# Kernel tuning notes

Measured on AMD Instinct MI355X. Metric: run time of the kernel, lower is better.

The kernel has to match this reference:

```python
import jax, jax.numpy as jnp
import numpy as np

N = 100000
E = 1600000
IN_C = 128
HID = 32
OUT_C = 32
HEADS = 4
NEG_SLOPE = 0.2


def setup_inputs() -> dict:
    key = jax.random.key(0)
    ks = jax.random.split(key, 8)
    x = jax.random.normal(ks[0], (N, IN_C), dtype=jnp.float32)
    edge_index = jax.random.randint(ks[1], (2, E), 0, N, dtype=jnp.int64)
    s = 0.1
    W1 = jax.random.normal(ks[2], (IN_C, HEADS * HID), dtype=jnp.float32) * s
    att_src1 = jax.random.normal(ks[3], (HEADS, HID), dtype=jnp.float32) * s
    att_dst1 = jax.random.normal(ks[4], (HEADS, HID), dtype=jnp.float32) * s
    W2 = jax.random.normal(ks[5], (HEADS * HID, HEADS * OUT_C), dtype=jnp.float32) * s
    att_src2 = jax.random.normal(ks[6], (HEADS, OUT_C), dtype=jnp.float32) * s
    att_dst2 = jax.random.normal(ks[7], (HEADS, OUT_C), dtype=jnp.float32) * s
    return {"x": x, "edge_index": edge_index, "W1": W1, "att_src1": att_src1,
            "att_dst1": att_dst1, "W2": W2, "att_src2": att_src2, "att_dst2": att_dst2}


def _gat_conv(x, src, dst, W, a_src, a_dst, heads, ch):
    # linear transform: [N, heads, ch]
    h = (x @ W).reshape(-1, heads, ch)
    # per-node attention logits [N, heads]
    al_src = jnp.sum(h * a_src, axis=-1)
    al_dst = jnp.sum(h * a_dst, axis=-1)
    # per-edge attention [E, heads]
    e = jax.nn.leaky_relu(al_src[src] + al_dst[dst], negative_slope=NEG_SLOPE)
    # segment softmax over incoming edges of each dst node
    m = jax.ops.segment_max(e, dst, num_segments=N)
    e = jnp.exp(e - m[dst])
    denom = jax.ops.segment_sum(e, dst, num_segments=N)
    alpha = e / (denom[dst] + 1e-16)
    # message + scatter-add aggregation
    msg = h[src] * alpha[:, :, None]          # [E, heads, ch]
    out = jax.ops.segment_sum(msg, dst, num_segments=N)
    return out.reshape(-1, heads * ch)        # concat heads (PyG default)


def reference(x, edge_index, W1, att_src1, att_dst1, W2, att_src2, att_dst2):
    # add self-loops (PyG GATConv default add_self_loops=True)
    loop = jnp.arange(N, dtype=edge_index.dtype)
    src = jnp.concatenate([edge_index[0], loop])
    dst = jnp.concatenate([edge_index[1], loop])
    h = _gat_conv(x, src, dst, W1, att_src1, att_dst1, HEADS, HID)
    h = jax.nn.relu(h)  # dropout is identity in eval mode
    out = _gat_conv(h, src, dst, W2, att_src2, att_dst2, HEADS, OUT_C)
    return out
```

## Files before the change

kernel.cpp:

```cpp
#include <hip/hip_runtime.h>

#define NN 100000
#define EE 1600000
#define NGRP 8
#define DRANGE 12500
#define SLOTS 48
#define NROWPAD 100032
#define NTILES 1563
#define PREP_BLK 50
#define BUILD_BLK 2048
#define GEMM_BLK 512

typedef short bf16x8 __attribute__((ext_vector_type(8)));
typedef float f32x4 __attribute__((ext_vector_type(4)));
typedef int   i32x4 __attribute__((ext_vector_type(4)));
typedef unsigned int u32x2 __attribute__((ext_vector_type(2)));

__device__ __forceinline__ float leaky(float x) { return x > 0.f ? x : 0.2f * x; }

__device__ __forceinline__ unsigned int bfpack2(float a, float b)
{
    unsigned int xa = __float_as_uint(a), xb = __float_as_uint(b);
    xa = (xa + 0x7fffu + ((xa >> 16) & 1u)) >> 16;
    xb = (xb + 0x7fffu + ((xb >> 16) & 1u)) & 0xffff0000u;
    return xa | xb;
}

__device__ __forceinline__ unsigned short bf1(float a)
{
    unsigned int x = __float_as_uint(a);
    return (unsigned short)((x + 0x7fffu + ((x >> 16) & 1u)) >> 16);
}

__device__ __forceinline__ float blo(unsigned int u) { return __uint_as_float(u << 16); }
__device__ __forceinline__ float bhi(unsigned int u) { return __uint_as_float(u & 0xffff0000u); }


__global__ __launch_bounds__(256) void prep_build(const float* __restrict__ W1, const float* __restrict__ W2,
                                                  unsigned short* __restrict__ Wtb1, unsigned short* __restrict__ Wtb2,
                                                  const float* __restrict__ as1, const float* __restrict__ ad1,
                                                  const float* __restrict__ as2, const float* __restrict__ ad2,
                                                  unsigned short* __restrict__ Wa1, unsigned short* __restrict__ Wa2,
                                                  unsigned int* __restrict__ Xbf,
                                                  const int* __restrict__ src, const int* __restrict__ dst,
                                                  int* __restrict__ cnt, int* __restrict__ csr)
{
    const int bid = blockIdx.x;
    if (bid < 32) {
        int tid = bid * 256 + threadIdx.x;
        int layer = tid >> 12;
        int rem = tid & 4095;
        int c = rem >> 5;
        int kq = (rem & 31) * 4;
        const float* Ws = layer ? W2 : W1;
        unsigned short* Wd = layer ? Wtb2 : Wtb1;
        ushort4 o;
        o.x = bf1(Ws[(kq + 0) * 128 + c]);
        o.y = bf1(Ws[(kq + 1) * 128 + c]);
        o.z = bf1(Ws[(kq + 2) * 128 + c]);
        o.w = bf1(Ws[(kq + 3) * 128 + c]);
        *(ushort4*)&Wd[c * 128 + kq] = o;
    } else if (bid < 48) {
        int tid = (bid - 32) * 256 + threadIdx.x;
        int layer = tid >> 11;
        int rem = tid & 2047;
        int col = rem >> 7;
        int k = rem & 127;
        const float* Ws = layer ? W2 : W1;
        unsigned short* Wd = layer ? Wa2 : Wa1;
        float s = 0.f;
        if (col < 8) {
            int head = col & 3;
            const float* av = (col < 4) ? (layer ? as2 : as1) : (layer ? ad2 : ad1);
            const float* wr = Ws + k * 128 + head * 32;
            const float* ar = av + head * 32;
            #pragma unroll
            for (int c = 0; c < 32; c++) s += wr[c] * ar[c];
        }
        Wd[col * 128 + k] = bf1(s);
    } else if (bid < PREP_BLK) {
        int t = (bid - 48) * 256 + threadIdx.x;
        ((uint4*)Xbf)[NN * 16 + t] = make_uint4(0, 0, 0, 0);
    } else {
        const int bb = bid - PREP_BLK;
        const int grp = bb & (NGRP - 1);
        const int gr  = bb >> 3;
        const int ng  = BUILD_BLK >> 3;
        const int dlo = grp * DRANGE, dhi = dlo + DRANGE;
        const int tid0 = gr * 256 + threadIdx.x;
        const int nthr = ng * 256;
        for (int e4 = tid0 * 4; e4 < EE; e4 += nthr * 4) {
            i32x4 dv = __builtin_nontemporal_load((const i32x4*)(dst + e4));
            i32x4 sv = __builtin_nontemporal_load((const i32x4*)(src + e4));
            #pragma unroll
            for (int j = 0; j < 4; ++j) {
                int d = dv[j];
                if (d >= dlo && d < dhi) {
                    int pos = atomicAdd(&cnt[d], 1);
                    if (pos < SLOTS) csr[(size_t)d * SLOTS + pos] = sv[j];
                }
            }
        }
    }
}


template<bool FP32IN>
__global__ __launch_bounds__(256) void gemm_mfma(const void* __restrict__ Xin,
                                                 const unsigned short* __restrict__ Wtb,
                                                 const unsigned short* __restrict__ Wa,
                                                 unsigned int* __restrict__ Hbf,
                                                 float* __restrict__ alS, float* __restrict__ alD)
{
    const int w = threadIdx.x >> 6, lane = threadIdx.x & 63;
    const int cl = lane & 15, b = lane >> 4;

    bf16x8 Bf[8][4];
    #pragma unroll
    for (int c = 0; c < 8; c++)
        #pragma unroll
        for (int s = 0; s < 4; s++)
            Bf[c][s] = *(const bf16x8*)(Wtb + (16 * c + cl) * 128 + 32 * s + 8 * b);

    bf16x8 Bf9[4];
    #pragma unroll
    for (int s = 0; s < 4; s++)
        Bf9[s] = *(const bf16x8*)(Wa + cl * 128 + 32 * s + 8 * b);

    for (int tile = blockIdx.x; tile < NTILES; tile += GEMM_BLK) {
        const int rowb = tile * 64 + 16 * w;
        const int rA = rowb + cl;
        bf16x8 Af[4];
        if constexpr (FP32IN) {
            if (rA < NN) {
                const float* pa = (const float*)Xin + (size_t)rA * 128 + 8 * b;
                #pragma unroll
                for (int s = 0; s < 4; s++) {
                    float4 f0 = *(const float4*)(pa + 32 * s);
                    float4 f1 = *(const float4*)(pa + 32 * s + 4);
                    union { bf16x8 v; unsigned int u[4]; } cv;
                    cv.u[0] = bfpack2(f0.x, f0.y); cv.u[1] = bfpack2(f0.z, f0.w);
                    cv.u[2] = bfpack2(f1.x, f1.y); cv.u[3] = bfpack2(f1.z, f1.w);
                    Af[s] = cv.v;
                }
            } else {
                union { bf16x8 v; unsigned int u[4]; } cz;
                cz.u[0] = cz.u[1] = cz.u[2] = cz.u[3] = 0;
                #pragma unroll
                for (int s = 0; s < 4; s++) Af[s] = cz.v;
            }
        } else {
            const unsigned short* pa = (const unsigned short*)Xin + (size_t)rA * 128 + 8 * b;
            #pragma unroll
            for (int s = 0; s < 4; s++) Af[s] = *(const bf16x8*)(pa + 32 * s);
        }

        f32x4 acc[8];
        #pragma unroll
        for (int c = 0; c < 8; c++) acc[c] = (f32x4){0.f, 0.f, 0.f, 0.f};
        f32x4 acc9 = (f32x4){0.f, 0.f, 0.f, 0.f};
        #pragma unroll
        for (int s = 0; s < 4; s++) {
            #pragma unroll
            for (int c = 0; c < 8; c++)
                acc[c] = __builtin_amdgcn_mfma_f32_16x16x32_bf16(Af[s], Bf[c][s], acc[c], 0, 0, 0);
            acc9 = __builtin_amdgcn_mfma_f32_16x16x32_bf16(Af[s], Bf9[s], acc9, 0, 0, 0);
        }

        const int row0 = rowb + 4 * b;
        #pragma unroll
        for (int c = 0; c < 8; c++) {
            #pragma unroll
            for (int r = 0; r < 4; r++) {
                float partner = __shfl_xor(acc[c][r], 1);
                if (!(cl & 1) && row0 + r < NN)
                    Hbf[(size_t)(row0 + r) * 64 + 8 * c + (cl >> 1)] = bfpack2(acc[c][r], partner);
            }
        }
        #pragma unroll
        for (int r = 0; r < 4; r++) {
            const int rr = row0 + r;
            if (rr < NN) {
                if (cl < 4)      alS[rr * 4 + cl] = acc9[r];
                else if (cl < 8) alD[rr * 4 + (cl - 4)] = acc9[r];
            }
        }
    }
}


__global__ __launch_bounds__(256) void agg_kernel(const unsigned int* __restrict__ Hbf,
                                                  const int* __restrict__ cnt, const int* __restrict__ csr,
                                                  const float* __restrict__ alS, const float* __restrict__ alD,
                                                  float* __restrict__ OUTf, unsigned int* __restrict__ OUTb,
                                                  int do_relu)
{
    __shared__ float pl[4][64 * 4];
    __shared__ int   sl[4][64];
    const int w = threadIdx.x >> 6, lane = threadIdx.x & 63;
    const int wid = (blockIdx.x * 256 + threadIdx.x) >> 6;
    if (wid >= NN) return;
    const int nreal = min(cnt[wid], SLOTS);
    const int nE = nreal + 1;
    const float4 ad = *(const float4*)&alD[wid * 4];
    const int half = lane >> 5, l5 = lane & 31;
    const int hq = l5 >> 3;
    const uint2* __restrict__ H2 = (const uint2*)Hbf + l5;
    const int* __restrict__ slots = csr + (size_t)wid * SLOTS;

    float4 acc = make_float4(0.f, 0.f, 0.f, 0.f);
    float den = 0.f;
    for (int base = 0; base < nE; base += 64) {
        const int nthis = min(64, nE - base);
        const int idx = base + lane;
        int s_ = 0;
        float4 p = make_float4(0.f, 0.f, 0.f, 0.f);
        if (lane < nthis) {
            s_ = (idx == nreal) ? wid : __builtin_nontemporal_load(slots + idx);
            float4 as = *(const float4*)&alS[s_ * 4];
            p.x = __expf(leaky(as.x + ad.x));
            p.y = __expf(leaky(as.y + ad.y));
            p.z = __expf(leaky(as.z + ad.z));
            p.w = __expf(leaky(as.w + ad.w));
        }
        sl[w][lane] = s_;
        *(float4*)&pl[w][lane * 4] = p;
        int k = 0;
        for (; k + 8 <= nthis; k += 8) {
            float p0 = pl[w][(k + half) * 4 + hq];
            float p1 = pl[w][(k + 2 + half) * 4 + hq];
            float p2 = pl[w][(k + 4 + half) * 4 + hq];
            float p3 = pl[w][(k + 6 + half) * 4 + hq];
            int s0i = sl[w][k + half];
            int s1i = sl[w][k + 2 + half];
            int s2i = sl[w][k + 4 + half];
            int s3i = sl[w][k + 6 + half];
            uint2 u0 = H2[(size_t)s0i * 32];
            uint2 u1 = H2[(size_t)s1i * 32];
            uint2 u2 = H2[(size_t)s2i * 32];
            uint2 u3 = H2[(size_t)s3i * 32];
            den += (p0 + p1) + (p2 + p3);
            acc.x += p0 * blo(u0.x); acc.y += p0 * bhi(u0.x);
            acc.z += p0 * blo(u0.y); acc.w += p0 * bhi(u0.y);
            acc.x += p1 * blo(u1.x); acc.y += p1 * bhi(u1.x);
            acc.z += p1 * blo(u1.y); acc.w += p1 * bhi(u1.y);
            acc.x += p2 * blo(u2.x); acc.y += p2 * bhi(u2.x);
            acc.z += p2 * blo(u2.y); acc.w += p2 * bhi(u2.y);
            acc.x += p3 * blo(u3.x); acc.y += p3 * bhi(u3.x);
            acc.z += p3 * blo(u3.y); acc.w += p3 * bhi(u3.y);
        }
        for (; k < nthis; k += 2) {
            float paf = pl[w][(k + half) * 4 + hq];
            int sa = sl[w][k + half];
            uint2 ua = H2[(size_t)sa * 32];
            den += paf;
            acc.x += paf * blo(ua.x); acc.y += paf * bhi(ua.x);
            acc.z += paf * blo(ua.y); acc.w += paf * bhi(ua.y);
        }
    }
    acc.x += __shfl_xor(acc.x, 32);
    acc.y += __shfl_xor(acc.y, 32);
    acc.z += __shfl_xor(acc.z, 32);
    acc.w += __shfl_xor(acc.w, 32);
    den   += __shfl_xor(den,   32);
    if (half == 0) {
        float inv = 1.f / (den + 1e-16f);
        float o0 = acc.x * inv, o1 = acc.y * inv, o2 = acc.z * inv, o3 = acc.w * inv;
        if (do_relu) {
            o0 = fmaxf(o0, 0.f); o1 = fmaxf(o1, 0.f);
            o2 = fmaxf(o2, 0.f); o3 = fmaxf(o3, 0.f);
        }
        if (OUTb) {
            u32x2 ov = { bfpack2(o0, o1), bfpack2(o2, o3) };
            __builtin_nontemporal_store(ov, (u32x2*)&OUTb[(size_t)wid * 64 + l5 * 2]);
        } else {
            f32x4 ov = { o0, o1, o2, o3 };
            __builtin_nontemporal_store(ov, (f32x4*)&OUTf[(size_t)wid * 128 + l5 * 4]);
        }
    }
}


extern "C" void kernel_launch(void* const* d_in, const int* in_sizes, int n_in,
                              void* d_out, int out_size, void* d_ws, size_t ws_size,
                              hipStream_t stream)
{
    const float* x   = (const float*)d_in[0];
    const int*   ei  = (const int*)d_in[1];
    const float* W1  = (const float*)d_in[2];
    const float* as1 = (const float*)d_in[3];
    const float* ad1 = (const float*)d_in[4];
    const float* W2  = (const float*)d_in[5];
    const float* as2 = (const float*)d_in[6];
    const float* ad2 = (const float*)d_in[7];
    const int* srcp = ei;
    const int* dstp = ei + EE;

    char* w = (char*)d_ws;
    unsigned int* Xbf  = (unsigned int*)w; w += (size_t)NROWPAD * 64 * 4;
    unsigned int* Hbf  = (unsigned int*)w; w += (size_t)NN * 64 * 4;
    unsigned short* Wtb1 = (unsigned short*)w; w += 16384 * 2;
    unsigned short* Wtb2 = (unsigned short*)w; w += 16384 * 2;
    unsigned short* Wa1  = (unsigned short*)w; w += 2048 * 2;
    unsigned short* Wa2  = (unsigned short*)w; w += 2048 * 2;
    float* alS = (float*)w; w += (size_t)NN * 4 * 4;
    float* alD = (float*)w; w += (size_t)NN * 4 * 4;
    int* cnt    = (int*)w;  w += (size_t)NN * 4;
    int* csr    = (int*)w;  w += (size_t)NN * SLOTS * 4;

    hipMemsetAsync(cnt, 0, NN * sizeof(int), stream);
    prep_build<<<PREP_BLK + BUILD_BLK, 256, 0, stream>>>(W1, W2, Wtb1, Wtb2,
                                                         as1, ad1, as2, ad2, Wa1, Wa2,
                                                         Xbf, srcp, dstp, cnt, csr);

    const int node_wave_blocks = (NN + 3) / 4;

    gemm_mfma<true><<<GEMM_BLK, 256, 0, stream>>>(x, Wtb1, Wa1, Hbf, alS, alD);
    agg_kernel<<<node_wave_blocks, 256, 0, stream>>>(Hbf, cnt, csr, alS, alD, nullptr, Xbf, 1);

    gemm_mfma<false><<<GEMM_BLK, 256, 0, stream>>>(Xbf, Wtb2, Wa2, Hbf, alS, alD);
    agg_kernel<<<node_wave_blocks, 256, 0, stream>>>(Hbf, cnt, csr, alS, alD, (float*)d_out, nullptr, 0);
}
```

Baseline: 288.9 us.

## Partition edges into destination buckets before CSR build; widen aggregation loads

The CSR build changes from each of 8 groups scanning all edges to a two-pass scheme. First, edges are partitioned into 8 destination-range buckets using shared-memory counters and one global atomic per bucket per block. A second kernel then fills the per-node slots from the bucketed edges. This cuts the 8x redundant reads of the edge list but adds an intermediate 64-bit edge buffer and an extra launch. Separately, the aggregation kernel now has each lane load 16 bytes (8 bf16 channels) with 4 edges in flight per wave, and it drops the outer loop beyond 64 edges, which assumes degree plus one never exceeds 64 (safe since SLOTS is 48).

```diff
diff --git a/kernel.cpp b/kernel.cpp
--- a/kernel.cpp
+++ b/kernel.cpp
@@ -8,13 +8,16 @@
 #define NROWPAD 100032
 #define NTILES 1563
 #define PREP_BLK 50
-#define BUILD_BLK 2048
+#define PART_BLK 512
+#define NITER 4
+#define EBCAP 225000
+#define BUILD2_BLK 2048
 #define GEMM_BLK 512
 
 typedef short bf16x8 __attribute__((ext_vector_type(8)));
 typedef float f32x4 __attribute__((ext_vector_type(4)));
 typedef int   i32x4 __attribute__((ext_vector_type(4)));
-typedef unsigned int u32x2 __attribute__((ext_vector_type(2)));
+typedef unsigned int u32x4 __attribute__((ext_vector_type(4)));
 
 __device__ __forceinline__ float leaky(float x) { return x > 0.f ? x : 0.2f * x; }
 
@@ -36,14 +39,14 @@
 __device__ __forceinline__ float bhi(unsigned int u) { return __uint_as_float(u & 0xffff0000u); }
 
 
-__global__ __launch_bounds__(256) void prep_build(const float* __restrict__ W1, const float* __restrict__ W2,
-                                                  unsigned short* __restrict__ Wtb1, unsigned short* __restrict__ Wtb2,
-                                                  const float* __restrict__ as1, const float* __restrict__ ad1,
-                                                  const float* __restrict__ as2, const float* __restrict__ ad2,
-                                                  unsigned short* __restrict__ Wa1, unsigned short* __restrict__ Wa2,
-                                                  unsigned int* __restrict__ Xbf,
-                                                  const int* __restrict__ src, const int* __restrict__ dst,
-                                                  int* __restrict__ cnt, int* __restrict__ csr)
+__global__ __launch_bounds__(256) void prep_part(const float* __restrict__ W1, const float* __restrict__ W2,
+                                                 unsigned short* __restrict__ Wtb1, unsigned short* __restrict__ Wtb2,
+                                                 const float* __restrict__ as1, const float* __restrict__ ad1,
+                                                 const float* __restrict__ as2, const float* __restrict__ ad2,
+                                                 unsigned short* __restrict__ Wa1, unsigned short* __restrict__ Wa2,
+                                                 unsigned int* __restrict__ Xbf,
+                                                 const int* __restrict__ src, const int* __restrict__ dst,
+                                                 int* __restrict__ bktcnt, unsigned long long* __restrict__ ebuf)
 {
     const int bid = blockIdx.x;
     if (bid < 32) {
@@ -82,25 +85,59 @@
         int t = (bid - 48) * 256 + threadIdx.x;
         ((uint4*)Xbf)[NN * 16 + t] = make_uint4(0, 0, 0, 0);
     } else {
+        __shared__ int lcnt[8];
+        __shared__ int lbase[8];
         const int bb = bid - PREP_BLK;
-        const int grp = bb & (NGRP - 1);
-        const int gr  = bb >> 3;
-        const int ng  = BUILD_BLK >> 3;
-        const int dlo = grp * DRANGE, dhi = dlo + DRANGE;
-        const int tid0 = gr * 256 + threadIdx.x;
-        const int nthr = ng * 256;
-        for (int e4 = tid0 * 4; e4 < EE; e4 += nthr * 4) {
-            i32x4 dv = __builtin_nontemporal_load((const i32x4*)(dst + e4));
-            i32x4 sv = __builtin_nontemporal_load((const i32x4*)(src + e4));
-            #pragma unroll
-            for (int j = 0; j < 4; ++j) {
-                int d = dv[j];
-                if (d >= dlo && d < dhi) {
-                    int pos = atomicAdd(&cnt[d], 1);
-                    if (pos < SLOTS) csr[(size_t)d * SLOTS + pos] = sv[j];
+        const int t = threadIdx.x;
+        const int nthr = PART_BLK * 256;
+        for (int it = 0; it < NITER; ++it) {
+            const int qidx = it * nthr + bb * 256 + t;
+            const bool valid = qidx < EE / 4;
+            if (t < 8) lcnt[t] = 0;
+            __syncthreads();
+            i32x4 dv, sv;
+            int g[4], pl_[4];
+            if (valid) {
+                dv = __builtin_nontemporal_load((const i32x4*)(dst + qidx * 4));
+                sv = __builtin_nontemporal_load((const i32x4*)(src + qidx * 4));
+                #pragma unroll
+                for (int j = 0; j < 4; ++j) {
+                    g[j] = dv[j] / DRANGE;
+                    pl_[j] = atomicAdd(&lcnt[g[j]], 1);
                 }
             }
-        }
+            __syncthreads();
+            if (t < 8) lbase[t] = atomicAdd(&bktcnt[t], lcnt[t]);
+            __syncthreads();
+            if (valid) {
+                #pragma unroll
+                for (int j = 0; j < 4; ++j) {
+                    int idx = lbase[g[j]] + pl_[j];
+                    ebuf[(size_t)g[j] * EBCAP + idx] =
+                        ((unsigned long long)(unsigned int)dv[j] << 32) | (unsigned int)sv[j];
+                }
+            }
+            __syncthreads();
+        }
+    }
+}
+
+
+__global__ __launch_bounds__(256) void build2_kernel(const int* __restrict__ bktcnt,
+                                                     const unsigned long long* __restrict__ ebuf,
+                                                     int* __restrict__ cnt, int* __restrict__ csr)
+{
+    const int g = blockIdx.x & (NGRP - 1);
+    const int gr = blockIdx.x >> 3;
+    const int ng = BUILD2_BLK >> 3;
+    const int n = bktcnt[g];
+    const unsigned long long* __restrict__ eb = ebuf + (size_t)g * EBCAP;
+    for (int i = gr * 256 + threadIdx.x; i < n; i += ng * 256) {
+        unsigned long long e = __builtin_nontemporal_load(eb + i);
+        int d = (int)(e >> 32);
+        int s = (int)(e & 0xffffffffu);
+        int pos = atomicAdd(&cnt[d], 1);
+        if (pos < SLOTS) csr[(size_t)d * SLOTS + pos] = s;
     }
 }
 
@@ -203,20 +240,19 @@
     const int nreal = min(cnt[wid], SLOTS);
     const int nE = nreal + 1;
     const float4 ad = *(const float4*)&alD[wid * 4];
-    const int half = lane >> 5, l5 = lane & 31;
-    const int hq = l5 >> 3;
-    const uint2* __restrict__ H2 = (const uint2*)Hbf + l5;
+    const int q = lane >> 4;
+    const int l4 = lane & 15;
+    const int hq = l4 >> 2;
+    const u32x4* __restrict__ H4 = (const u32x4*)Hbf + l4;
     const int* __restrict__ slots = csr + (size_t)wid * SLOTS;
 
-    float4 acc = make_float4(0.f, 0.f, 0.f, 0.f);
+    float a0 = 0.f, a1 = 0.f, a2 = 0.f, a3 = 0.f, a4 = 0.f, a5 = 0.f, a6 = 0.f, a7 = 0.f;
     float den = 0.f;
-    for (int base = 0; base < nE; base += 64) {
-        const int nthis = min(64, nE - base);
-        const int idx = base + lane;
+    {
         int s_ = 0;
         float4 p = make_float4(0.f, 0.f, 0.f, 0.f);
-        if (lane < nthis) {
-            s_ = (idx == nreal) ? wid : __builtin_nontemporal_load(slots + idx);
+        if (lane < nE) {
+            s_ = (lane == nreal) ? wid : __builtin_nontemporal_load(slots + lane);
             float4 as = *(const float4*)&alS[s_ * 4];
             p.x = __expf(leaky(as.x + ad.x));
             p.y = __expf(leaky(as.y + ad.y));
@@ -226,56 +262,61 @@
         sl[w][lane] = s_;
         *(float4*)&pl[w][lane * 4] = p;
         int k = 0;
-        for (; k + 8 <= nthis; k += 8) {
-            float p0 = pl[w][(k + half) * 4 + hq];
-            float p1 = pl[w][(k + 2 + half) * 4 + hq];
-            float p2 = pl[w][(k + 4 + half) * 4 + hq];
-            float p3 = pl[w][(k + 6 + half) * 4 + hq];
-            int s0i = sl[w][k + half];
-            int s1i = sl[w][k + 2 + half];
-            int s2i = sl[w][k + 4 + half];
-            int s3i = sl[w][k + 6 + half];
-            uint2 u0 = H2[(size_t)s0i * 32];
-            uint2 u1 = H2[(size_t)s1i * 32];
-            uint2 u2 = H2[(size_t)s2i * 32];
-            uint2 u3 = H2[(size_t)s3i * 32];
-            den += (p0 + p1) + (p2 + p3);
-            acc.x += p0 * blo(u0.x); acc.y += p0 * bhi(u0.x);
-            acc.z += p0 * blo(u0.y); acc.w += p0 * bhi(u0.y);
-            acc.x += p1 * blo(u1.x); acc.y += p1 * bhi(u1.x);
-            acc.z += p1 * blo(u1.y); acc.w += p1 * bhi(u1.y);
-            acc.x += p2 * blo(u2.x); acc.y += p2 * bhi(u2.x);
-            acc.z += p2 * blo(u2.y); acc.w += p2 * bhi(u2.y);
-            acc.x += p3 * blo(u3.x); acc.y += p3 * bhi(u3.x);
-            acc.z += p3 * blo(u3.y); acc.w += p3 * bhi(u3.y);
-        }
-        for (; k < nthis; k += 2) {
-            float paf = pl[w][(k + half) * 4 + hq];
-            int sa = sl[w][k + half];
-            uint2 ua = H2[(size_t)sa * 32];
-            den += paf;
-            acc.x += paf * blo(ua.x); acc.y += paf * bhi(ua.x);
-            acc.z += paf * blo(ua.y); acc.w += paf * bhi(ua.y);
-        }
-    }
-    acc.x += __shfl_xor(acc.x, 32);
-    acc.y += __shfl_xor(acc.y, 32);
-    acc.z += __shfl_xor(acc.z, 32);
-    acc.w += __shfl_xor(acc.w, 32);
-    den   += __shfl_xor(den,   32);
-    if (half == 0) {
+        for (; k + 16 <= nE; k += 16) {
+            float pA = pl[w][(k + q) * 4 + hq];
+            float pB = pl[w][(k + 4 + q) * 4 + hq];
+            float pC = pl[w][(k + 8 + q) * 4 + hq];
+            float pD = pl[w][(k + 12 + q) * 4 + hq];
+            int sA = sl[w][k + q];
+            int sB = sl[w][k + 4 + q];
+            int sC = sl[w][k + 8 + q];
+            int sD = sl[w][k + 12 + q];
+            u32x4 uA = H4[(size_t)sA * 16];
+            u32x4 uB = H4[(size_t)sB * 16];
+            u32x4 uC = H4[(size_t)sC * 16];
+            u32x4 uD = H4[(size_t)sD * 16];
+            den += (pA + pB) + (pC + pD);
+            a0 += pA * blo(uA.x); a1 += pA * bhi(uA.x); a2 += pA * blo(uA.y); a3 += pA * bhi(uA.y);
+            a4 += pA * blo(uA.z); a5 += pA * bhi(uA.z); a6 += pA * blo(uA.w); a7 += pA * bhi(uA.w);
+            a0 += pB * blo(uB.x); a1 += pB * bhi(uB.x); a2 += pB * blo(uB.y); a3 += pB * bhi(uB.y);
+            a4 += pB * blo(uB.z); a5 += pB * bhi(uB.z); a6 += pB * blo(uB.w); a7 += pB * bhi(uB.w);
+            a0 += pC * blo(uC.x); a1 += pC * bhi(uC.x); a2 += pC * blo(uC.y); a3 += pC * bhi(uC.y);
+            a4 += pC * blo(uC.z); a5 += pC * bhi(uC.z); a6 += pC * blo(uC.w); a7 += pC * bhi(uC.w);
+            a0 += pD * blo(uD.x); a1 += pD * bhi(uD.x); a2 += pD * blo(uD.y); a3 += pD * bhi(uD.y);
+            a4 += pD * blo(uD.z); a5 += pD * bhi(uD.z); a6 += pD * blo(uD.w); a7 += pD * bhi(uD.w);
+        }
+        for (; k < nE; k += 4) {
+            float pA = pl[w][(k + q) * 4 + hq];
+            int sA = sl[w][k + q];
+            u32x4 uA = H4[(size_t)sA * 16];
+            den += pA;
+            a0 += pA * blo(uA.x); a1 += pA * bhi(uA.x); a2 += pA * blo(uA.y); a3 += pA * bhi(uA.y);
+            a4 += pA * blo(uA.z); a5 += pA * bhi(uA.z); a6 += pA * blo(uA.w); a7 += pA * bhi(uA.w);
+        }
+    }
+    #pragma unroll
+    for (int off = 16; off <= 32; off <<= 1) {
+        a0 += __shfl_xor(a0, off); a1 += __shfl_xor(a1, off);
+        a2 += __shfl_xor(a2, off); a3 += __shfl_xor(a3, off);
+        a4 += __shfl_xor(a4, off); a5 += __shfl_xor(a5, off);
+        a6 += __shfl_xor(a6, off); a7 += __shfl_xor(a7, off);
+        den += __shfl_xor(den, off);
+    }
+    if (q == 0) {
         float inv = 1.f / (den + 1e-16f);
-        float o0 = acc.x * inv, o1 = acc.y * inv, o2 = acc.z * inv, o3 = acc.w * inv;
+        a0 *= inv; a1 *= inv; a2 *= inv; a3 *= inv;
+        a4 *= inv; a5 *= inv; a6 *= inv; a7 *= inv;
         if (do_relu) {
-            o0 = fmaxf(o0, 0.f); o1 = fmaxf(o1, 0.f);
-            o2 = fmaxf(o2, 0.f); o3 = fmaxf(o3, 0.f);
+            a0 = fmaxf(a0, 0.f); a1 = fmaxf(a1, 0.f); a2 = fmaxf(a2, 0.f); a3 = fmaxf(a3, 0.f);
+            a4 = fmaxf(a4, 0.f); a5 = fmaxf(a5, 0.f); a6 = fmaxf(a6, 0.f); a7 = fmaxf(a7, 0.f);
         }
         if (OUTb) {
-            u32x2 ov = { bfpack2(o0, o1), bfpack2(o2, o3) };
-            __builtin_nontemporal_store(ov, (u32x2*)&OUTb[(size_t)wid * 64 + l5 * 2]);
+            u32x4 ov = { bfpack2(a0, a1), bfpack2(a2, a3), bfpack2(a4, a5), bfpack2(a6, a7) };
+            __builtin_nontemporal_store(ov, (u32x4*)OUTb + (size_t)wid * 16 + l4);
         } else {
-            f32x4 ov = { o0, o1, o2, o3 };
-            __builtin_nontemporal_store(ov, (f32x4*)&OUTf[(size_t)wid * 128 + l5 * 4]);
+            f32x4 o0 = {a0, a1, a2, a3}, o1 = {a4, a5, a6, a7};
+            __builtin_nontemporal_store(o0, (f32x4*)&OUTf[(size_t)wid * 128 + l4 * 8]);
+            __builtin_nontemporal_store(o1, (f32x4*)&OUTf[(size_t)wid * 128 + l4 * 8 + 4]);
         }
     }
 }
@@ -306,12 +347,15 @@
     float* alS = (float*)w; w += (size_t)NN * 4 * 4;
     float* alD = (float*)w; w += (size_t)NN * 4 * 4;
     int* cnt    = (int*)w;  w += (size_t)NN * 4;
+    int* bktcnt = (int*)w;  w += 8 * 4;
     int* csr    = (int*)w;  w += (size_t)NN * SLOTS * 4;
-
-    hipMemsetAsync(cnt, 0, NN * sizeof(int), stream);
-    prep_build<<<PREP_BLK + BUILD_BLK, 256, 0, stream>>>(W1, W2, Wtb1, Wtb2,
-                                                         as1, ad1, as2, ad2, Wa1, Wa2,
-                                                         Xbf, srcp, dstp, cnt, csr);
+    unsigned long long* ebuf = (unsigned long long*)w; w += (size_t)NGRP * EBCAP * 8;
+
+    (void)hipMemsetAsync(cnt, 0, (NN + 8) * sizeof(int), stream);
+    prep_part<<<PREP_BLK + PART_BLK, 256, 0, stream>>>(W1, W2, Wtb1, Wtb2,
+                                                       as1, ad1, as2, ad2, Wa1, Wa2,
+                                                       Xbf, srcp, dstp, bktcnt, ebuf);
+    build2_kernel<<<BUILD2_BLK, 256, 0, stream>>>(bktcnt, ebuf, cnt, csr);
 
     const int node_wave_blocks = (NN + 3) / 4;
 
```

Result: slower. 310.5 us (+7.5%).
